# Kernel tuning notes

Hardware: AMD Instinct MI355X
Metric: run time of the kernel (lower is better)

The kernel has to match this reference:

```python
import jax, jax.numpy as jnp
import numpy as np

T, R, D, N = 26, 100000, 128, 10   # tables, rows/table, embed width, nnz per bag
B, NUM = 16384, 13                 # batch, numerical features
MLP = [1024, 512, 256]


def setup_inputs() -> dict:
    key = jax.random.key(0)
    ks = jax.random.split(key, 12)
    tables = jax.random.normal(ks[0], (T, R, D), jnp.float32) * 0.01
    numerical = jax.random.normal(ks[1], (B, NUM), jnp.float32)
    cat = jax.random.randint(ks[2], (B, T, N), 0, R, dtype=jnp.int32)
    dims_in = [T * D + NUM] + MLP
    dims_out = MLP + [1]
    out = {"numerical": numerical, "cat": cat, "tables": tables}
    for i, (din, dout) in enumerate(zip(dims_in, dims_out)):
        out[f"W{i}"] = jax.random.normal(ks[3 + i], (din, dout), jnp.float32) * (1.0 / np.sqrt(din))
        out[f"b{i}"] = jnp.zeros((dout,), jnp.float32)
    return out


def reference(numerical, cat, tables, W0, b0, W1, b1, W2, b2, W3, b3):
    # Multi-hot embedding-bag with sum combiner, per table.
    # tables: [T,R,D], cat: [B,T,N] -> emb: [B,T,D]
    bag = jax.vmap(lambda tab, ix: tab[ix].sum(axis=1), in_axes=(0, 1), out_axes=1)
    emb = bag(tables, cat)                                  # [B,T,D]
    x = jnp.concatenate([emb.reshape(emb.shape[0], -1), numerical], axis=1)  # [B, T*D+NUM]
    for W, b in ((W0, b0), (W1, b1), (W2, b2)):
        x = jax.nn.relu(x @ W + b)
    return x @ W3 + b3                                      # [B,1]
```

## Files before the change

### kernel.cpp

```cpp
#include <hip/hip_runtime.h>

#define TT   26
#define RR   100000
#define DD   128
#define NN   10
#define BB   16384
#define NUMF 13
#define KP0  3392

typedef __bf16 bf16x8 __attribute__((ext_vector_type(8)));
typedef float  f32x4  __attribute__((ext_vector_type(4)));
typedef unsigned int u32x2 __attribute__((ext_vector_type(2)));

__device__ __forceinline__ unsigned short f2bf(float f) {
    unsigned int u = __float_as_uint(f);
    u += 0x7FFFu + ((u >> 16) & 1u);
    return (unsigned short)(u >> 16);
}

__device__ __forceinline__ void gload_lds16(const void* g, void* l) {
    __builtin_amdgcn_global_load_lds(
        (const __attribute__((address_space(1))) void*)g,
        (__attribute__((address_space(3))) void*)l, 16, 0, 0);
}

__global__ __launch_bounds__(256) void transpose_cvt(
    const float* __restrict__ in, unsigned short* __restrict__ out,
    int Kin, int KPad, int N)
{
    __shared__ float tile[64][65];
    int k0 = blockIdx.x * 64;
    int n0 = blockIdx.y * 64;
    int c  = threadIdx.x & 63;
    int rr = threadIdx.x >> 6;
    #pragma unroll
    for (int r = rr; r < 64; r += 4) {
        int k = k0 + r, n = n0 + c;
        float v = 0.f;
        if (k < Kin && n < N) v = in[(size_t)k * N + n];
        tile[r][c] = v;
    }
    __syncthreads();
    #pragma unroll
    for (int r = rr; r < 64; r += 4) {
        int n = n0 + r, kp = k0 + c;
        if (n < N && kp < KPad)
            out[(size_t)n * KPad + kp] = f2bf(tile[c][r]);
    }
}

__global__ __launch_bounds__(256) void embed_bag(
    const float* __restrict__ tables, const int* __restrict__ cat,
    unsigned short* __restrict__ x)
{
    int wid  = blockIdx.x * 4 + (threadIdx.x >> 6);
    int lane = threadIdx.x & 63;
    int t = wid >> 14;
    int b = wid & (BB - 1);
    const int* ip = cat + ((size_t)b * TT + t) * NN;
    const float* tbase = tables + (size_t)t * RR * DD;
    int half = lane >> 5;
    int l5   = lane & 31;
    f32x4 acc = {0.f, 0.f, 0.f, 0.f};
    #pragma unroll
    for (int n2 = 0; n2 < 5; n2++) {
        int r = __builtin_nontemporal_load(ip + 2 * n2 + half);
        f32x4 v = *(const f32x4*)(tbase + (size_t)r * DD + l5 * 4);
        acc += v;
    }
    float t0 = acc[0] + __shfl_xor(acc[0], 32, 64);
    float t1 = acc[1] + __shfl_xor(acc[1], 32, 64);
    float t2 = acc[2] + __shfl_xor(acc[2], 32, 64);
    float t3 = acc[3] + __shfl_xor(acc[3], 32, 64);
    if (half == 0) {
        u32x2 pk;
        pk[0] = (unsigned int)f2bf(t0) | ((unsigned int)f2bf(t1) << 16);
        pk[1] = (unsigned int)f2bf(t2) | ((unsigned int)f2bf(t3) << 16);
        __builtin_nontemporal_store(pk, (u32x2*)(x + (size_t)b * KP0 + t * DD + l5 * 4));
    }
}

__global__ __launch_bounds__(256) void num_fill(
    const float* __restrict__ numerical, unsigned short* __restrict__ x)
{
    int b    = blockIdx.x * 4 + (threadIdx.x >> 6);
    int lane = threadIdx.x & 63;
    unsigned short v = 0;
    if (lane < NUMF) v = f2bf(numerical[b * NUMF + lane]);
    __builtin_nontemporal_store(v, x + (size_t)b * KP0 + TT * DD + lane);
}

__device__ __forceinline__ void stage_tile(
    const unsigned short* __restrict__ src,
    unsigned short* lds, int K, int k0, int tid)
{
    #pragma unroll
    for (int j = 0; j < 4; j++) {
        int ch = j * 256 + tid;
        const unsigned short* g = src + (size_t)(ch >> 3) * K + k0 + (ch & 7) * 8;
        gload_lds16(g, lds + (size_t)(j * 256 + (tid & 192)) * 8);
    }
}

__global__ __launch_bounds__(256) void gemm_bias_relu(
    const unsigned short* __restrict__ A,
    const unsigned short* __restrict__ Bt,
    const float* __restrict__ bias,
    unsigned short* __restrict__ C,
    int M, int N, int K, int do_relu)
{
    __shared__ __align__(16) unsigned short As[128 * 64];
    __shared__ __align__(16) unsigned short Bs[128 * 64];

    const int tid  = threadIdx.x;
    const int lane = tid & 63;
    const int w    = tid >> 6;
    const int wm   = w >> 1, wn = w & 1;

    int nwg  = gridDim.x * gridDim.y;
    int orig = blockIdx.y * gridDim.x + blockIdx.x;
    int cpx  = nwg >> 3;
    int swz  = (orig & 7) * cpx + (orig >> 3);
    int bx   = swz % gridDim.x;
    int by   = swz / gridDim.x;
    const int m0 = by * 128, n0 = bx * 128;

    f32x4 acc[4][4];
    #pragma unroll
    for (int i = 0; i < 4; i++)
        #pragma unroll
        for (int j = 0; j < 4; j++) {
            f32x4 z = {0.f, 0.f, 0.f, 0.f};
            acc[i][j] = z;
        }

    const unsigned short* Abase = A  + (size_t)m0 * K;
    const unsigned short* Bbase = Bt + (size_t)n0 * K;

    for (int k0 = 0; k0 < K; k0 += 64) {
        stage_tile(Abase, As, K, k0, tid);
        stage_tile(Bbase, Bs, K, k0, tid);
        __syncthreads();
        #pragma unroll
        for (int kk = 0; kk < 2; kk++) {
            bf16x8 af[4], bfv[4];
            #pragma unroll
            for (int mi = 0; mi < 4; mi++) {
                int off = (wm * 64 + mi * 16 + (lane & 15)) * 64 + kk * 32 + (lane >> 4) * 8;
                af[mi] = *(const bf16x8*)(As + off);
            }
            #pragma unroll
            for (int ni = 0; ni < 4; ni++) {
                int off = (wn * 64 + ni * 16 + (lane & 15)) * 64 + kk * 32 + (lane >> 4) * 8;
                bfv[ni] = *(const bf16x8*)(Bs + off);
            }
            #pragma unroll
            for (int mi = 0; mi < 4; mi++)
                #pragma unroll
                for (int ni = 0; ni < 4; ni++)
                    acc[mi][ni] = __builtin_amdgcn_mfma_f32_16x16x32_bf16(
                        af[mi], bfv[ni], acc[mi][ni], 0, 0, 0);
        }
        __syncthreads();
    }

    #pragma unroll
    for (int mi = 0; mi < 4; mi++) {
        int row_base = m0 + wm * 64 + mi * 16 + (lane >> 4) * 4;
        #pragma unroll
        for (int ni = 0; ni < 4; ni++) {
            int col = n0 + wn * 64 + ni * 16 + (lane & 15);
            float bv = bias[col];
            #pragma unroll
            for (int j = 0; j < 4; j++) {
                float v = acc[mi][ni][j] + bv;
                if (do_relu) v = v > 0.f ? v : 0.f;
                C[(size_t)(row_base + j) * N + col] = f2bf(v);
            }
        }
    }
}

__global__ __launch_bounds__(256) void final_dot(
    const unsigned short* __restrict__ h3, const float* __restrict__ W3,
    const float* __restrict__ b3, float* __restrict__ out)
{
    int b    = blockIdx.x * 4 + (threadIdx.x >> 6);
    int lane = threadIdx.x & 63;
    uint2 u = *(const uint2*)(h3 + (size_t)b * 256 + lane * 4);
    float f0 = __uint_as_float((u.x & 0xffffu) << 16);
    float f1 = __uint_as_float(u.x & 0xffff0000u);
    float f2 = __uint_as_float((u.y & 0xffffu) << 16);
    float f3 = __uint_as_float(u.y & 0xffff0000u);
    float4 wv = *(const float4*)(W3 + lane * 4);
    float s = f0 * wv.x + f1 * wv.y + f2 * wv.z + f3 * wv.w;
    #pragma unroll
    for (int off = 32; off > 0; off >>= 1) s += __shfl_down(s, off, 64);
    if (lane == 0) out[b] = s + b3[0];
}

extern "C" void kernel_launch(void* const* d_in, const int* in_sizes, int n_in,
                              void* d_out, int out_size, void* d_ws, size_t ws_size,
                              hipStream_t stream)
{
    const float* numerical = (const float*)d_in[0];
    const int*   cat       = (const int*)d_in[1];
    const float* tables    = (const float*)d_in[2];
    const float* W0 = (const float*)d_in[3];
    const float* b0 = (const float*)d_in[4];
    const float* W1 = (const float*)d_in[5];
    const float* b1 = (const float*)d_in[6];
    const float* W2 = (const float*)d_in[7];
    const float* b2 = (const float*)d_in[8];
    const float* W3 = (const float*)d_in[9];
    const float* b3 = (const float*)d_in[10];
    float* out = (float*)d_out;

    unsigned short* x   = (unsigned short*)d_ws;
    unsigned short* w0t = x   + (size_t)BB * KP0;
    unsigned short* w1t = w0t + (size_t)1024 * KP0;
    unsigned short* w2t = w1t + (size_t)512 * 1024;
    unsigned short* h1  = w2t + (size_t)256 * 512;
    unsigned short* h2  = x;
    unsigned short* h3  = x   + (size_t)BB * 512;

    transpose_cvt<<<dim3(53, 16), 256, 0, stream>>>(W0, w0t, TT * DD + NUMF, KP0, 1024);
    transpose_cvt<<<dim3(16, 8),  256, 0, stream>>>(W1, w1t, 1024, 1024, 512);
    transpose_cvt<<<dim3(8, 4),   256, 0, stream>>>(W2, w2t, 512, 512, 256);

    embed_bag<<<dim3(BB * TT / 4), 256, 0, stream>>>(tables, cat, x);
    num_fill <<<dim3(BB / 4),      256, 0, stream>>>(numerical, x);

    gemm_bias_relu<<<dim3(8, 128), 256, 0, stream>>>(x,  w0t, b0, h1, BB, 1024, KP0, 1);
    gemm_bias_relu<<<dim3(4, 128), 256, 0, stream>>>(h1, w1t, b1, h2, BB, 512, 1024, 1);
    gemm_bias_relu<<<dim3(2, 128), 256, 0, stream>>>(h2, w2t, b2, h3, BB, 256, 512, 1);

    final_dot<<<dim3(BB / 4), 256, 0, stream>>>(h3, W3, b3, out);
}
```

Baseline: 581.7 us.

## Replace first MLP GEMM with 256x256-tile, 4-buffer pipelined MFMA kernel

Measured after the change: 516.1 us. 1.13x faster.

```diff
diff --git a/kernel.cpp b/kernel.cpp
--- a/kernel.cpp
+++ b/kernel.cpp
@@ -88,6 +88,117 @@
     unsigned short v = 0;
     if (lane < NUMF) v = f2bf(numerical[b * NUMF + lane]);
     __builtin_nontemporal_store(v, x + (size_t)b * KP0 + TT * DD + lane);
+}
+
+#define G_BUFB 32768
+
+__global__ __launch_bounds__(512, 2) void gemm256(
+    const unsigned short* __restrict__ A,
+    const unsigned short* __restrict__ Bt,
+    const float* __restrict__ bias,
+    unsigned short* __restrict__ C,
+    int M, int N, int K, int do_relu)
+{
+    extern __shared__ __align__(16) char lds[];
+    const int tid  = threadIdx.x;
+    const int lane = tid & 63;
+    const int w    = tid >> 6;
+    const int wm   = w >> 2, wn = w & 3;
+
+    int nwg  = gridDim.x * gridDim.y;
+    int orig = blockIdx.y * gridDim.x + blockIdx.x;
+    int cpx  = nwg >> 3;
+    int swz  = (orig & 7) * cpx + (orig >> 3);
+    int bx   = swz % gridDim.x;
+    int by   = swz / gridDim.x;
+    const int m0 = by * 256, n0 = bx * 256;
+
+    const int NT = K >> 5;
+
+    f32x4 acc[8][4];
+    #pragma unroll
+    for (int i = 0; i < 8; i++)
+        #pragma unroll
+        for (int j = 0; j < 4; j++) {
+            f32x4 z = {0.f, 0.f, 0.f, 0.f};
+            acc[i][j] = z;
+        }
+
+    auto stage_unit = [&](int h, int u) {
+        int i    = ((u & 1) << 9) + tid;
+        int row  = 2 * (i >> 3) + ((i >> 2) & 1);
+        int col8 = i & 3;
+        const unsigned short* base = (u < 2)
+            ? (A  + (size_t)(m0 + row) * K)
+            : (Bt + (size_t)(n0 + row) * K);
+        const unsigned short* g = base + (h << 5) + col8 * 8;
+        char* l = lds + (size_t)(h & 3) * G_BUFB + ((u >> 1) << 14) + ((u & 1) << 13)
+                      + ((tid >> 6) << 10);
+        gload_lds16(g, l);
+    };
+
+    #pragma unroll
+    for (int u = 0; u < 4; u++) stage_unit(0, u);
+    #pragma unroll
+    for (int u = 0; u < 4; u++) stage_unit(1, u);
+    asm volatile("s_waitcnt vmcnt(4)" ::: "memory");
+    __builtin_amdgcn_s_barrier();
+
+    for (int h = 0; h < NT; ++h) {
+        const char* bufR = lds + (size_t)(h & 3) * G_BUFB;
+        const bool  do_stage = (h + 2) < NT;
+
+        bf16x8 bfr[4];
+        #pragma unroll
+        for (int p = 0; p < 4; p++) {
+            if (do_stage) stage_unit(h + 2, p);
+            if (p == 0) {
+                #pragma unroll
+                for (int nf = 0; nf < 4; nf++) {
+                    int r = wn * 64 + nf * 16 + (lane & 15);
+                    bfr[nf] = *(const bf16x8*)(bufR + 16384 + ((r >> 1) << 7)
+                                               + ((r & 1) << 6) + ((lane >> 4) << 4));
+                }
+            }
+            bf16x8 afr[2];
+            #pragma unroll
+            for (int q = 0; q < 2; q++) {
+                int r = wm * 128 + (2 * p + q) * 16 + (lane & 15);
+                afr[q] = *(const bf16x8*)(bufR + ((r >> 1) << 7)
+                                          + ((r & 1) << 6) + ((lane >> 4) << 4));
+            }
+            asm volatile("s_waitcnt lgkmcnt(0)" ::: "memory");
+            __builtin_amdgcn_sched_barrier(0);
+            __builtin_amdgcn_s_setprio(1);
+            #pragma unroll
+            for (int q = 0; q < 2; q++)
+                #pragma unroll
+                for (int nf = 0; nf < 4; nf++)
+                    acc[2 * p + q][nf] = __builtin_amdgcn_mfma_f32_16x16x32_bf16(
+                        afr[q], bfr[nf], acc[2 * p + q][nf], 0, 0, 0);
+            __builtin_amdgcn_s_setprio(0);
+            if (p < 3) __builtin_amdgcn_s_barrier();
+        }
+        if (do_stage) asm volatile("s_waitcnt vmcnt(4)" ::: "memory");
+        else          asm volatile("s_waitcnt vmcnt(0)" ::: "memory");
+        __builtin_amdgcn_s_barrier();
+    }
+
+    #pragma unroll
+    for (int mf = 0; mf < 8; mf++) {
+        int row_base = m0 + wm * 128 + mf * 16 + (lane >> 4) * 4;
+        #pragma unroll
+        for (int nf = 0; nf < 4; nf++) {
+            int col = n0 + wn * 64 + nf * 16 + (lane & 15);
+            float bv = bias[col];
+            #pragma unroll
+            for (int j = 0; j < 4; j++) {
+                float v = acc[mf][nf][j] + bv;
+                if (do_relu) v = v > 0.f ? v : 0.f;
+                C[(size_t)(row_base + j) * N + col] = f2bf(v);
+            }
+        }
+    }
 }
 
 __device__ __forceinline__ void stage_tile(
@@ -224,6 +335,9 @@
     unsigned short* h2  = x;
     unsigned short* h3  = x   + (size_t)BB * 512;
 
+    (void)hipFuncSetAttribute((const void*)gemm256,
+                              hipFuncAttributeMaxDynamicSharedMemorySize, 131072);
+
     transpose_cvt<<<dim3(53, 16), 256, 0, stream>>>(W0, w0t, TT * DD + NUMF, KP0, 1024);
     transpose_cvt<<<dim3(16, 8),  256, 0, stream>>>(W1, w1t, 1024, 1024, 512);
     transpose_cvt<<<dim3(8, 4),   256, 0, stream>>>(W2, w2t, 512, 512, 256);
@@ -231,7 +345,8 @@
     embed_bag<<<dim3(BB * TT / 4), 256, 0, stream>>>(tables, cat, x);
     num_fill <<<dim3(BB / 4),      256, 0, stream>>>(numerical, x);
 
-    gemm_bias_relu<<<dim3(8, 128), 256, 0, stream>>>(x,  w0t, b0, h1, BB, 1024, KP0, 1);
+    gemm256<<<dim3(1024 / 256, BB / 256), 512, 131072, stream>>>(
+        x, w0t, b0, h1, BB, 1024, KP0, 1);
     gemm_bias_relu<<<dim3(4, 128), 256, 0, stream>>>(h1, w1t, b1, h2, BB, 512, 1024, 1);
     gemm_bias_relu<<<dim3(2, 128), 256, 0, stream>>>(h2, w2t, b2, h3, BB, 256, 512, 1);
 
```
